# Performance work log

Measured on AMD Instinct MI355X. Metric: run time of the kernel, lower is better.

Reference implementation:

```python
import jax, jax.numpy as jnp
import numpy as np

D_MODEL = 128
D_INNER = 256   # expand=2
D_STATE = 16
DT_RANK = 8     # ceil(128/16)
D_CONV = 2
GROUPS = 4
EPS = 1e-5


def _mamba_dir(x, W_in, conv_w, conv_b, W_x, W_dt, b_dt, A_log, D, W_out):
    # x: [B, L, d_model]
    B, L, _ = x.shape
    xz = x @ W_in                               # [B, L, 2*d_inner]
    xp, z = xz[..., :D_INNER], xz[..., D_INNER:]
    # depthwise causal conv, kernel size 2 (pad-left 1)
    xprev = jnp.pad(xp, ((0, 0), (1, 0), (0, 0)))[:, :L]
    xc = jax.nn.silu(xprev * conv_w[:, 0] + xp * conv_w[:, 1] + conv_b)
    xdb = xc @ W_x                              # [B, L, dt_rank + 2*d_state]
    dt_r = xdb[..., :DT_RANK]
    Bc = xdb[..., DT_RANK:DT_RANK + D_STATE]    # [B, L, d_state]
    Cc = xdb[..., DT_RANK + D_STATE:]           # [B, L, d_state]
    dt = jax.nn.softplus(dt_r @ W_dt + b_dt)    # [B, L, d_inner]
    A = -jnp.exp(A_log)                         # [d_inner, d_state]

    def step(h, inp):
        dt_t, B_t, C_t, x_t = inp               # [B,di], [B,ds], [B,ds], [B,di]
        dA = jnp.exp(dt_t[:, :, None] * A)      # [B, di, ds]
        h = dA * h + (dt_t * x_t)[:, :, None] * B_t[:, None, :]
        y = jnp.einsum('bds,bs->bd', h, C_t)
        return h, y

    h0 = jnp.zeros((B, D_INNER, D_STATE), x.dtype)
    xs = (jnp.moveaxis(dt, 1, 0), jnp.moveaxis(Bc, 1, 0),
          jnp.moveaxis(Cc, 1, 0), jnp.moveaxis(xc, 1, 0))
    _, ys = jax.lax.scan(step, h0, xs)          # ys: [L, B, d_inner]
    y = jnp.moveaxis(ys, 0, 1) + D * xc
    y = y * jax.nn.silu(z)
    return y @ W_out                            # [B, L, d_model]


def _groupnorm_silu(x, gamma, beta):
    B, C, H, W = x.shape
    xg = x.reshape(B, GROUPS, C // GROUPS, H, W)
    mu = xg.mean(axis=(2, 3, 4), keepdims=True)
    var = xg.var(axis=(2, 3, 4), keepdims=True)
    xn = ((xg - mu) * jax.lax.rsqrt(var + EPS)).reshape(B, C, H, W)
    return jax.nn.silu(xn * gamma[None, :, None, None] + beta[None, :, None, None])


def setup_inputs() -> dict:
    key = jax.random.key(0)
    ks = jax.random.split(key, 24)
    s = 0.02
    A_log = jnp.log(jnp.tile(jnp.arange(1, D_STATE + 1, dtype=jnp.float32)[None, :], (D_INNER, 1)))
    inp = {"x": jax.random.normal(ks[0], (4, D_MODEL, 64, 64), jnp.float32)}
    for i, sfx in enumerate(("f", "b")):
        o = 1 + 9 * i
        inp[f"W_in_{sfx}"] = jax.random.normal(ks[o], (D_MODEL, 2 * D_INNER)) * s
        inp[f"conv_w_{sfx}"] = jax.random.normal(ks[o + 1], (D_INNER, D_CONV)) * 0.5
        inp[f"conv_b_{sfx}"] = jnp.zeros((D_INNER,))
        inp[f"W_x_{sfx}"] = jax.random.normal(ks[o + 2], (D_INNER, DT_RANK + 2 * D_STATE)) * s
        inp[f"W_dt_{sfx}"] = jax.random.normal(ks[o + 3], (DT_RANK, D_INNER)) * s
        inp[f"b_dt_{sfx}"] = jnp.full((D_INNER,), -3.0)
        inp[f"A_log_{sfx}"] = A_log
        inp[f"D_{sfx}"] = jnp.ones((D_INNER,))
        inp[f"W_out_{sfx}"] = jax.random.normal(ks[o + 4], (D_INNER, D_MODEL)) * s
    inp["gn_gamma"] = jnp.ones((D_MODEL,))
    inp["gn_beta"] = jnp.zeros((D_MODEL,))
    return inp


def reference(x, W_in_f, conv_w_f, conv_b_f, W_x_f, W_dt_f, b_dt_f, A_log_f, D_f, W_out_f,
              W_in_b, conv_w_b, conv_b_b, W_x_b, W_dt_b, b_dt_b, A_log_b, D_b, W_out_b,
              gn_gamma, gn_beta):
    B, C, H, W = x.shape
    xs = x.transpose(0, 2, 3, 1).reshape(B, H * W, C)
    y_f = _mamba_dir(xs, W_in_f, conv_w_f, conv_b_f, W_x_f, W_dt_f, b_dt_f, A_log_f, D_f, W_out_f)
    xr = xs[:, ::-1]
    y_b = _mamba_dir(xr, W_in_b, conv_w_b, conv_b_b, W_x_b, W_dt_b, b_dt_b, A_log_b, D_b, W_out_b)[:, ::-1]
    y = y_f + y_b                               # bidirectional combine
    y = y.reshape(B, H, W, C).transpose(0, 3, 1, 2)
    y = _groupnorm_silu(y, gn_gamma, gn_beta)
    return y + x
```

## Files before the change

kernel.cpp:

```cpp
#include <hip/hip_runtime.h>

#define Bn 4
#define Ln 4096
#define Cn 128
#define DIn 256
#define NCn 128
#define LCn 32
#define ROWS (Bn*Ln)

typedef short s8v __attribute__((ext_vector_type(8)));
typedef short s4v __attribute__((ext_vector_type(4)));
typedef unsigned short u8v __attribute__((ext_vector_type(8)));
typedef unsigned short u4v __attribute__((ext_vector_type(4)));
typedef float f4v __attribute__((ext_vector_type(4)));
typedef float f2v __attribute__((ext_vector_type(2)));

__device__ __forceinline__ float siluf(float x){ return x / (1.f + __expf(-x)); }
__device__ __forceinline__ unsigned short bfr(float f){
  uint u = __float_as_uint(f);
  return (unsigned short)((u + 0x7fffu + ((u>>16)&1u)) >> 16);
}
__device__ __forceinline__ float bf2f(unsigned short u){ return __uint_as_float(((uint)u)<<16); }

__device__ __forceinline__ void sp_w(float r, float& dtv, float& w){
  float e = __expf(-fabsf(r));
  float rc = 1.f / (1.f + e);
  dtv = fmaxf(r, 0.f) + __logf(1.f + e);
  w = (r > 0.f) ? e * rc : rc;
}

__device__ __forceinline__ int tile_off(int r, int gran, int ghalf){
  return ((r>>4)<<9) + ((r&15)<<5) + (((gran ^ ((r>>1)&3)))<<3) + ghalf;
}

#define SMEMB 18432

__global__ __launch_bounds__(256) void k_g1(const float* __restrict__ x,
    const float* __restrict__ Wf, const float* __restrict__ Wb,
    unsigned short* __restrict__ xpf, unsigned short* __restrict__ xpb,
    unsigned short* __restrict__ zbf, unsigned short* __restrict__ zbb)
{
  const int dir = blockIdx.z;
  const float* __restrict__ W = dir ? Wb : Wf;
  unsigned short* __restrict__ xp = dir ? xpb : xpf;
  unsigned short* __restrict__ zb = dir ? zbb : zbf;
  const int row0 = blockIdx.x * 128;
  const int n0 = blockIdx.y;
  const int b = row0 >> 12;
  const int t0 = row0 & (Ln-1);
  const float* __restrict__ xb = x + (size_t)b * Cn * Ln;

  __shared__ __align__(16) char smem[SMEMB];
  short* Ast = (short*)smem;
  short* Bst = (short*)smem + 8*512;
  float* Te  = (float*)smem;

  const int tid = threadIdx.x;
  const int lane = tid & 63;
  const int wid = tid >> 6;
  const int wr = wid >> 1, wc = wid & 1;
  const int r16 = lane & 15, kg = lane >> 4;

  const int q = tid & 31, kq = tid >> 5;
  const int kbase = 4*kq;
  const int g_true = kq >> 1;
  const int ghalf = (kq & 1) * 4;

  f4v acc[4][4];
  #pragma unroll
  for (int i=0;i<4;++i)
    #pragma unroll
    for (int j=0;j<4;++j) acc[i][j] = (f4v){0.f,0.f,0.f,0.f};

  float4 va[4], vb[4];
  {
    #pragma unroll
    for (int kk=0;kk<4;++kk) {
      va[kk] = (dir==0)
        ? *(const float4*)(xb + (size_t)(kbase+kk)*Ln + t0 + 4*q)
        : *(const float4*)(xb + (size_t)(kbase+kk)*Ln + (Ln-4 - t0 - 4*q));
      vb[kk] = *(const float4*)(W + (size_t)(kbase+kk)*512 + n0*128 + 4*q);
    }
  }
  for (int ks=0; ks<4; ++ks) {
    if (ks) __syncthreads();
    #pragma unroll
    for (int e=0;e<4;++e) {
      int r = 4*q + e;
      int off = tile_off(r, g_true, ghalf);
      int c = dir ? (3-e) : e;
      s4v hv;
      #pragma unroll
      for (int kk=0;kk<4;++kk) hv[kk] = (short)bfr(((const float*)&va[kk])[c]);
      *(s4v*)&Ast[off] = hv;
    }
    #pragma unroll
    for (int e=0;e<4;++e) {
      int r = 4*q + e;
      int off = tile_off(r, g_true, ghalf);
      s4v hv;
      #pragma unroll
      for (int kk=0;kk<4;++kk) hv[kk] = (short)bfr(((const float*)&vb[kk])[e]);
      *(s4v*)&Bst[off] = hv;
    }
    __syncthreads();
    if (ks < 3) {
      const int k0n = (ks+1)*32;
      #pragma unroll
      for (int kk=0;kk<4;++kk) {
        va[kk] = (dir==0)
          ? *(const float4*)(xb + (size_t)(k0n+kbase+kk)*Ln + t0 + 4*q)
          : *(const float4*)(xb + (size_t)(k0n+kbase+kk)*Ln + (Ln-4 - t0 - 4*q));
        vb[kk] = *(const float4*)(W + (size_t)(k0n+kbase+kk)*512 + n0*128 + 4*q);
      }
    }
    const int gsh = ((kg ^ ((r16>>1)&3)) << 3);
    s8v fa[4], fb[4];
    #pragma unroll
    for (int m=0;m<4;++m) fa[m] = *(const s8v*)&Ast[(wr*4+m)*512 + r16*32 + gsh];
    #pragma unroll
    for (int n=0;n<4;++n) fb[n] = *(const s8v*)&Bst[(wc*4+n)*512 + r16*32 + gsh];
    #pragma unroll
    for (int m=0;m<4;++m)
      #pragma unroll
      for (int n=0;n<4;++n)
        acc[m][n] = __builtin_amdgcn_mfma_f32_16x16x32_bf16(fa[m], fb[n], acc[m][n], 0,0,0);
  }
  __syncthreads();
  float* Tw = Te + wid*1088;
  #pragma unroll
  for (int m=0;m<4;++m) {
    #pragma unroll
    for (int n=0;n<4;++n)
      #pragma unroll
      for (int v=0;v<4;++v)
        Tw[(kg*4+v)*68 + n*16 + r16] = acc[m][n][v];
    #pragma unroll
    for (int rr=0;rr<4;++rr) {
      int r = rr*4 + (lane>>4);
      int c4 = lane & 15;
      float4 v4 = *(const float4*)&Tw[r*68 + c4*4];
      int row = row0 + wr*64 + m*16 + r;
      int colL = wc*64 + c4*4;
      u4v u; u[0]=bfr(v4.x); u[1]=bfr(v4.y); u[2]=bfr(v4.z); u[3]=bfr(v4.w);
      if (n0 < 2) {
        *(u4v*)(xp + (size_t)row*256 + n0*128 + colL) = u;
      } else {
        *(u4v*)(zb + (size_t)row*256 + (n0-2)*128 + colL) = u;
      }
    }
  }
}

__global__ __launch_bounds__(256) void k_conv(
    const unsigned short* __restrict__ xpf, const unsigned short* __restrict__ xpb,
    const float* __restrict__ cwf, const float* __restrict__ cwb,
    const float* __restrict__ cbf, const float* __restrict__ cbb,
    unsigned short* __restrict__ xcf, unsigned short* __restrict__ xcb)
{
  const int dir = blockIdx.y;
  const unsigned short* __restrict__ xpd = dir ? xpb : xpf;
  const float* __restrict__ cw = dir ? cwb : cwf;
  const float* __restrict__ cb = dir ? cbb : cbf;
  unsigned short* __restrict__ xc = dir ? xcb : xcf;
  const int n4 = ROWS * 64;
  for (int idx4 = blockIdx.x*256 + threadIdx.x; idx4 < n4; idx4 += gridDim.x*256) {
    int row = idx4 >> 6;
    int d0 = (idx4 & 63) * 4;
    u4v curu = *(const u4v*)(xpd + (size_t)row*256 + d0);
    u4v prevu = (u4v){0,0,0,0};
    if (row & (Ln-1)) prevu = *(const u4v*)(xpd + (size_t)(row-1)*256 + d0);
    float4 cwA = *(const float4*)(cw + d0*2);
    float4 cwB = *(const float4*)(cw + d0*2 + 4);
    float4 cb4 = *(const float4*)(cb + d0);
    u4v r;
    r[0] = bfr(siluf(fmaf(bf2f(prevu[0]),cwA.x, fmaf(bf2f(curu[0]),cwA.y, cb4.x))));
    r[1] = bfr(siluf(fmaf(bf2f(prevu[1]),cwA.z, fmaf(bf2f(curu[1]),cwA.w, cb4.y))));
    r[2] = bfr(siluf(fmaf(bf2f(prevu[2]),cwB.x, fmaf(bf2f(curu[2]),cwB.y, cb4.z))));
    r[3] = bfr(siluf(fmaf(bf2f(prevu[3]),cwB.z, fmaf(bf2f(curu[3]),cwB.w, cb4.w))));
    *(u4v*)(xc + (size_t)row*256 + d0) = r;
  }
}

__global__ __launch_bounds__(256) void k_g2(
    const unsigned short* __restrict__ xcf, const unsigned short* __restrict__ xcb,
    const float* __restrict__ Wxf, const float* __restrict__ Wxb,
    float* __restrict__ xdbf, float* __restrict__ xdbb)
{
  const int dir = blockIdx.z;
  const unsigned short* __restrict__ xc = dir ? xcb : xcf;
  const float* __restrict__ Wx = dir ? Wxb : Wxf;
  float* __restrict__ xdb = dir ? xdbb : xdbf;
  const int row0 = blockIdx.x * 64;

  __shared__ __align__(16) short Ast[4*512];
  __shared__ __align__(16) short Bst[4*512];

  const int tid = threadIdx.x;
  const int lane = tid & 63;
  const int wid = tid >> 6;
  const int wr = wid >> 1, wc = wid & 1;
  const int r16 = lane & 15, kg = lane >> 4;
  const int ar = tid >> 2, ag = tid & 3;
  const int bn = tid & 63, bg = tid >> 6;

  f4v acc[2][2];
  #pragma unroll
  for (int i=0;i<2;++i)
    #pragma unroll
    for (int j=0;j<2;++j) acc[i][j] = (f4v){0.f,0.f,0.f,0.f};

  for (int ks=0; ks<8; ++ks) {
    const int k0 = ks*32;
    if (ks) __syncthreads();
    {
      u8v u = *(const u8v*)(xc + (size_t)(row0+ar)*256 + k0 + ag*8);
      *(u8v*)&Ast[tile_off(ar, ag, 0)] = u;
    }
    {
      s8v hv;
      #pragma unroll
      for (int i=0;i<8;++i) {
        int k = k0 + bg*8 + i;
        float f = (bn < 40) ? Wx[(size_t)k*40 + bn] : 0.f;
        hv[i] = (short)bfr(f);
      }
      *(s8v*)&Bst[tile_off(bn, bg, 0)] = hv;
    }
    __syncthreads();
    const int gsh = ((kg ^ ((r16>>1)&3)) << 3);
    s8v fa[2], fb[2];
    #pragma unroll
    for (int m=0;m<2;++m) fa[m] = *(const s8v*)&Ast[(wr*2+m)*512 + r16*32 + gsh];
    #pragma unroll
    for (int n=0;n<2;++n) fb[n] = *(const s8v*)&Bst[(wc*2+n)*512 + r16*32 + gsh];
    #pragma unroll
    for (int m=0;m<2;++m)
      #pragma unroll
      for (int n=0;n<2;++n)
        acc[m][n] = __builtin_amdgcn_mfma_f32_16x16x32_bf16(fa[m], fb[n], acc[m][n], 0,0,0);
  }
  #pragma unroll
  for (int m=0;m<2;++m)
    #pragma unroll
    for (int n=0;n<2;++n) {
      int col = wc*32 + n*16 + r16;
      if (col < 40) {
        #pragma unroll
        for (int v=0;v<4;++v) {
          int row = row0 + wr*32 + m*16 + kg*4 + v;
          xdb[(size_t)row*40 + col] = acc[m][n][v];
        }
      }
    }
}

__global__ __launch_bounds__(128,4) void k_pass1(
    const float* __restrict__ xdbf, const float* __restrict__ xdbb,
    const unsigned short* __restrict__ xcf, const unsigned short* __restrict__ xcb,
    const float* __restrict__ Wdtf, const float* __restrict__ Wdtb,
    const float* __restrict__ bdtf, const float* __restrict__ bdtb,
    const float* __restrict__ Alf, const float* __restrict__ Alb,
    float* __restrict__ sdtf, float* __restrict__ sdtb,
    float* __restrict__ hkf, float* __restrict__ hkb)
{
  const int dir = blockIdx.y;
  const float* __restrict__ xdb = dir ? xdbb : xdbf;
  const unsigned short* __restrict__ xc = dir ? xcb : xcf;
  const float* __restrict__ Wdt = dir ? Wdtb : Wdtf;
  const float* __restrict__ bdt = dir ? bdtb : bdtf;
  const float* __restrict__ Al  = dir ? Alb  : Alf;
  float* __restrict__ sdt = dir ? sdtb : sdtf;
  float* __restrict__ hk  = dir ? hkb  : hkf;
  const int dh = blockIdx.x & 1;
  const int cc = blockIdx.x >> 1;
  const int b = cc >> 7, c = cc & 127;
  const int t0 = c * LCn;
  __shared__ float S[LCn*32];
  const int tid = threadIdx.x;
  #pragma unroll
  for (int j=0;j<6;++j) {
    int idx = tid + j*128;
    int t = idx/24, jj = idx - t*24;
    S[t*32 + jj] = xdb[(size_t)(b*Ln + t0 + t)*40 + jj];
  }
  const int d = dh*128 + tid;
  float Areg[16];
  bool st = true;
  #pragma unroll
  for (int s=0;s<16;++s) {
    Areg[s] = -__expf(Al[d*16+s]);
    st = st && (fabsf(Areg[s] + (float)(s+1)) <= 3e-5f*(float)(s+1));
  }
  f2v wdt2[4];
  #pragma unroll
  for (int j=0;j<4;++j) wdt2[j] = (f2v){Wdt[(2*j)*256+d], Wdt[(2*j+1)*256+d]};
  const float bd = bdt[d];
  f2v h2[8];
  #pragma unroll
  for (int i=0;i<8;++i) h2[i] = (f2v){0.f,0.f};
  float sacc = 0.f;
  const unsigned short* xcp = xc + (size_t)(b*Ln + t0)*256 + d;
  __syncthreads();
  if (st) {
    for (int t=0;t<LCn;++t) {
      float4 sA = *(const float4*)&S[t*32];
      float4 sB = *(const float4*)&S[t*32+4];
      f2v r2 = (f2v){sA.x,sA.y}*wdt2[0] + (f2v){sA.z,sA.w}*wdt2[1];
      r2 = (f2v){sB.x,sB.y}*wdt2[2] + r2;
      r2 = (f2v){sB.z,sB.w}*wdt2[3] + r2;
      float rr = bd + r2.x + r2.y;
      float dtv, wv;
      sp_w(rr, dtv, wv);
      float4 b0 = *(const float4*)&S[t*32+8];
      float4 b1 = *(const float4*)&S[t*32+12];
      float4 b2 = *(const float4*)&S[t*32+16];
      float4 b3 = *(const float4*)&S[t*32+20];
      float xv = bf2f(xcp[(size_t)t*256]);
      float u = dtv * xv;
      sacc += dtv;
      float w2s = wv*wv;
      float w4 = w2s*w2s, w8 = w4*w4;
      f2v wstep = (f2v){w2s, w2s};
      f2v wpa = (f2v){wv, w2s};
      f2v wpb = wpa * (f2v){w8, w8};
      f2v u2 = (f2v){u, u};
      h2[0] = h2[0]*wpa + u2*(f2v){b0.x,b0.y}; wpa *= wstep;
      h2[4] = h2[4]*wpb + u2*(f2v){b2.x,b2.y}; wpb *= wstep;
      h2[1] = h2[1]*wpa + u2*(f2v){b0.z,b0.w}; wpa *= wstep;
      h2[5] = h2[5]*wpb + u2*(f2v){b2.z,b2.w}; wpb *= wstep;
      h2[2] = h2[2]*wpa + u2*(f2v){b1.x,b1.y}; wpa *= wstep;
      h2[6] = h2[6]*wpb + u2*(f2v){b3.x,b3.y}; wpb *= wstep;
      h2[3] = h2[3]*wpa + u2*(f2v){b1.z,b1.w};
      h2[7] = h2[7]*wpb + u2*(f2v){b3.z,b3.w};
    }
  } else {
    for (int t=0;t<LCn;++t) {
      float4 sA = *(const float4*)&S[t*32];
      float4 sB = *(const float4*)&S[t*32+4];
      float rr = bd;
      rr = fmaf(sA.x,wdt2[0].x, fmaf(sA.y,wdt2[0].y, fmaf(sA.z,wdt2[1].x, fmaf(sA.w,wdt2[1].y, rr))));
      rr = fmaf(sB.x,wdt2[2].x, fmaf(sB.y,wdt2[2].y, fmaf(sB.z,wdt2[3].x, fmaf(sB.w,wdt2[3].y, rr))));
      float dtv, wv;
      sp_w(rr, dtv, wv);
      float bq[16];
      #pragma unroll
      for (int i=0;i<4;++i) *(float4*)&bq[4*i] = *(const float4*)&S[t*32 + 8 + 4*i];
      float xv = bf2f(xcp[(size_t)t*256]);
      float u = dtv * xv;
      sacc += dtv;
      #pragma unroll
      for (int s=0;s<16;++s) {
        float hv = (s&1) ? h2[s>>1].y : h2[s>>1].x;
        hv = fmaf(hv, __expf(dtv*Areg[s]), u*bq[s]);
        if (s&1) h2[s>>1].y = hv; else h2[s>>1].x = hv;
      }
    }
  }
  sdt[(size_t)(b*NCn + c)*256 + d] = sacc;
  #pragma unroll
  for (int i=0;i<8;++i) {
    hk[(size_t)((b*NCn + c)*16 + 2*i)*256 + d]   = h2[i].x;
    hk[(size_t)((b*NCn + c)*16 + 2*i+1)*256 + d] = h2[i].y;
  }
}

__global__ __launch_bounds__(256) void k_pass2(
    const float* __restrict__ Alf, const float* __restrict__ Alb,
    const float* __restrict__ sdtf, const float* __restrict__ sdtb,
    float* __restrict__ hkf, float* __restrict__ hkb)
{
  const int dir = blockIdx.y;
  const float* __restrict__ Al  = dir ? Alb : Alf;
  const float* __restrict__ sdt = dir ? sdtb : sdtf;
  float* __restrict__ hk = dir ? hkb : hkf;
  int g = blockIdx.x*256 + threadIdx.x;
  int d = g & 255, s = (g >> 8) & 15, b = g >> 12;
  float Ad = -__expf(Al[d*16+s]);
  float h = 0.f;
  float sd_n = sdt[(size_t)(b*NCn)*256 + d];
  size_t hi_n = (size_t)((b*NCn)*16 + s)*256 + d;
  float he_n = hk[hi_n];
  for (int c=0;c<NCn;++c) {
    float sd = sd_n, he = he_n;
    size_t hi = hi_n;
    if (c+1 < NCn) {
      int bc = b*NCn + c + 1;
      sd_n = sdt[(size_t)bc*256 + d];
      hi_n = (size_t)(bc*16 + s)*256 + d;
      he_n = hk[hi_n];
    }
    hk[hi] = h;
    h = fmaf(__expf(Ad*sd), h, he);
  }
}

__global__ __launch_bounds__(128,4) void k_pass3(
    const float* __restrict__ xdbf, const float* __restrict__ xdbb,
    const unsigned short* __restrict__ xcf, const unsigned short* __restrict__ xcb,
    const float* __restrict__ Wdtf, const float* __restrict__ Wdtb,
    const float* __restrict__ bdtf, const float* __restrict__ bdtb,
    const float* __restrict__ Alf, const float* __restrict__ Alb,
    const float* __restrict__ Dvf, const float* __restrict__ Dvb,
    const float* __restrict__ hkf, const float* __restrict__ hkb,
    const unsigned short* __restrict__ zbf, const unsigned short* __restrict__ zbb,
    unsigned short* __restrict__ ygf, unsigned short* __restrict__ ygb)
{
  const int dir = blockIdx.y;
  const float* __restrict__ xdb = dir ? xdbb : xdbf;
  const unsigned short* __restrict__ xc = dir ? xcb : xcf;
  const float* __restrict__ Wdt = dir ? Wdtb : Wdtf;
  const float* __restrict__ bdt = dir ? bdtb : bdtf;
  const float* __restrict__ Al  = dir ? Alb  : Alf;
  const float* __restrict__ Dv  = dir ? Dvb  : Dvf;
  const float* __restrict__ hk  = dir ? hkb  : hkf;
  const unsigned short* __restrict__ zbd = dir ? zbb : zbf;
  unsigned short* __restrict__ yg = dir ? ygb : ygf;
  const int dh = blockIdx.x & 1;
  const int cc = blockIdx.x >> 1;
  const int b = cc >> 7, c = cc & 127;
  const int t0 = c * LCn;
  __shared__ float S[LCn*48];
  const int tid = threadIdx.x;
  #pragma unroll
  for (int j=0;j<10;++j) {
    int idx = tid + j*128;
    int t = idx/40, jj = idx - t*40;
    S[t*48 + jj] = xdb[(size_t)(b*Ln + t0 + t)*40 + jj];
  }
  const int d = dh*128 + tid;
  float Areg[16];
  bool st = true;
  #pragma unroll
  for (int s=0;s<16;++s) {
    Areg[s] = -__expf(Al[d*16+s]);
    st = st && (fabsf(Areg[s] + (float)(s+1)) <= 3e-5f*(float)(s+1));
  }
  f2v wdt2[4];
  #pragma unroll
  for (int j=0;j<4;++j) wdt2[j] = (f2v){Wdt[(2*j)*256+d], Wdt[(2*j+1)*256+d]};
  const float bd = bdt[d];
  const float Dd = Dv[d];
  f2v h2[8];
  #pragma unroll
  for (int i=0;i<8;++i)
    h2[i] = (f2v){hk[(size_t)((b*NCn + c)*16 + 2*i)*256 + d],
                  hk[(size_t)((b*NCn + c)*16 + 2*i+1)*256 + d]};
  const unsigned short* xcp = xc + (size_t)(b*Ln + t0)*256 + d;
  const unsigned short* zbp = zbd + (size_t)(b*Ln + t0)*256 + d;
  unsigned short* ygp = yg + (size_t)(b*Ln + t0)*256 + d;
  __syncthreads();
  if (st) {
    for (int t=0;t<LCn;++t) {
      float4 sA = *(const float4*)&S[t*48];
      float4 sB = *(const float4*)&S[t*48+4];
      f2v r2 = (f2v){sA.x,sA.y}*wdt2[0] + (f2v){sA.z,sA.w}*wdt2[1];
      r2 = (f2v){sB.x,sB.y}*wdt2[2] + r2;
      r2 = (f2v){sB.z,sB.w}*wdt2[3] + r2;
      float rr = bd + r2.x + r2.y;
      float dtv, wv;
      sp_w(rr, dtv, wv);
      float4 b0 = *(const float4*)&S[t*48+8];
      float4 b1 = *(const float4*)&S[t*48+12];
      float4 b2 = *(const float4*)&S[t*48+16];
      float4 b3 = *(const float4*)&S[t*48+20];
      float4 c0 = *(const float4*)&S[t*48+24];
      float4 c1 = *(const float4*)&S[t*48+28];
      float4 c2 = *(const float4*)&S[t*48+32];
      float4 c3 = *(const float4*)&S[t*48+36];
      float xv = bf2f(xcp[(size_t)t*256]);
      float u = dtv * xv;
      float w2s = wv*wv;
      float w4 = w2s*w2s, w8 = w4*w4;
      f2v wstep = (f2v){w2s, w2s};
      f2v wpa = (f2v){wv, w2s};
      f2v wpb = wpa * (f2v){w8, w8};
      f2v u2 = (f2v){u, u};
      f2v yA = (f2v){0.f,0.f}, yB = (f2v){0.f,0.f};
      h2[0] = h2[0]*wpa + u2*(f2v){b0.x,b0.y}; yA = h2[0]*(f2v){c0.x,c0.y} + yA; wpa *= wstep;
      h2[4] = h2[4]*wpb + u2*(f2v){b2.x,b2.y}; yB = h2[4]*(f2v){c2.x,c2.y} + yB; wpb *= wstep;
      h2[1] = h2[1]*wpa + u2*(f2v){b0.z,b0.w}; yA = h2[1]*(f2v){c0.z,c0.w} + yA; wpa *= wstep;
      h2[5] = h2[5]*wpb + u2*(f2v){b2.z,b2.w}; yB = h2[5]*(f2v){c2.z,c2.w} + yB; wpb *= wstep;
      h2[2] = h2[2]*wpa + u2*(f2v){b1.x,b1.y}; yA = h2[2]*(f2v){c1.x,c1.y} + yA; wpa *= wstep;
      h2[6] = h2[6]*wpb + u2*(f2v){b3.x,b3.y}; yB = h2[6]*(f2v){c3.x,c3.y} + yB; wpb *= wstep;
      h2[3] = h2[3]*wpa + u2*(f2v){b1.z,b1.w}; yA = h2[3]*(f2v){c1.z,c1.w} + yA;
      h2[7] = h2[7]*wpb + u2*(f2v){b3.z,b3.w}; yB = h2[7]*(f2v){c3.z,c3.w} + yB;
      float y = yA.x + yA.y + yB.x + yB.y;
      y = fmaf(Dd, xv, y);
      float zv = bf2f(zbp[(size_t)t*256]);
      ygp[(size_t)t*256] = bfr(y * siluf(zv));
    }
  } else {
    for (int t=0;t<LCn;++t) {
      float4 sA = *(const float4*)&S[t*48];
      float4 sB = *(const float4*)&S[t*48+4];
      float rr = bd;
      rr = fmaf(sA.x,wdt2[0].x, fmaf(sA.y,wdt2[0].y, fmaf(sA.z,wdt2[1].x, fmaf(sA.w,wdt2[1].y, rr))));
      rr = fmaf(sB.x,wdt2[2].x, fmaf(sB.y,wdt2[2].y, fmaf(sB.z,wdt2[3].x, fmaf(sB.w,wdt2[3].y, rr))));
      float dtv, wv;
      sp_w(rr, dtv, wv);
      float bq[16], cq[16];
      #pragma unroll
      for (int i=0;i<4;++i) {
        *(float4*)&bq[4*i] = *(const float4*)&S[t*48 + 8 + 4*i];
        *(float4*)&cq[4*i] = *(const float4*)&S[t*48 + 24 + 4*i];
      }
      float xv = bf2f(xcp[(size_t)t*256]);
      float u = dtv * xv;
      float y = 0.f;
      #pragma unroll
      for (int s=0;s<16;++s) {
        float hv = (s&1) ? h2[s>>1].y : h2[s>>1].x;
        hv = fmaf(hv, __expf(dtv*Areg[s]), u*bq[s]);
        if (s&1) h2[s>>1].y = hv; else h2[s>>1].x = hv;
        y = fmaf(hv, cq[s], y);
      }
      y = fmaf(Dd, xv, y);
      float zv = bf2f(zbp[(size_t)t*256]);
      ygp[(size_t)t*256] = bfr(y * siluf(zv));
    }
  }
}

__global__ __launch_bounds__(256) void k_gout(
    const unsigned short* __restrict__ ygf, const unsigned short* __restrict__ ygb,
    const float* __restrict__ Wof, const float* __restrict__ Wob,
    float* __restrict__ yp)
{
  const int row0 = blockIdx.x * 64;
  const int khalf = blockIdx.y;
  float* __restrict__ ypart = yp + (size_t)khalf * ROWS * 128;
  const int b = row0 >> 12;
  const int l0 = row0 & (Ln-1);

  __shared__ __align__(16) char smem[SMEMB];
  short* Ast = (short*)smem;
  short* Bst = (short*)smem + 4*512;
  float* Te  = (float*)smem;

  const int tid = threadIdx.x;
  const int lane = tid & 63;
  const int wid = tid >> 6;
  const int wr = wid >> 1, wc = wid & 1;
  const int r16 = lane & 15, kg = lane >> 4;

  const int ar = tid >> 2, ag = tid & 3;
  const int q = tid & 31, kq = tid >> 5;
  const int kbase = 4*kq;
  const int g_true = kq >> 1;
  const int ghalf = (kq & 1) * 4;

  f4v acc[2][4];
  #pragma unroll
  for (int i=0;i<2;++i)
    #pragma unroll
    for (int j=0;j<4;++j) acc[i][j] = (f4v){0.f,0.f,0.f,0.f};

  for (int ks=0; ks<8; ++ks) {
    const int dir = ks >> 2;
    const int kk0 = khalf*128 + (ks & 3)*32;
    const unsigned short* __restrict__ ygd = dir ? ygb : ygf;
    const float* __restrict__ Wod = dir ? Wob : Wof;
    if (ks) __syncthreads();
    {
      int rl = l0 + ar;
      size_t srow = (size_t)b*Ln + (dir ? (Ln-1-rl) : rl);
      u8v u = *(const u8v*)(ygd + srow*256 + kk0 + ag*8);
      *(u8v*)&Ast[tile_off(ar, ag, 0)] = u;
    }
    {
      float4 vb[4];
      #pragma unroll
      for (int kk=0;kk<4;++kk)
        vb[kk] = *(const float4*)(Wod + (size_t)(kk0+kbase+kk)*128 + 4*q);
      #pragma unroll
      for (int e=0;e<4;++e) {
        int r = 4*q + e;
        int off = tile_off(r, g_true, ghalf);
        s4v hv;
        #pragma unroll
        for (int kk=0;kk<4;++kk) hv[kk] = (short)bfr(((const float*)&vb[kk])[e]);
        *(s4v*)&Bst[off] = hv;
      }
    }
    __syncthreads();
    const int gsh = ((kg ^ ((r16>>1)&3)) << 3);
    s8v fa[2], fb[4];
    #pragma unroll
    for (int m=0;m<2;++m) fa[m] = *(const s8v*)&Ast[(wr*2+m)*512 + r16*32 + gsh];
    #pragma unroll
    for (int n=0;n<4;++n) fb[n] = *(const s8v*)&Bst[(wc*4+n)*512 + r16*32 + gsh];
    #pragma unroll
    for (int m=0;m<2;++m)
      #pragma unroll
      for (int n=0;n<4;++n)
        acc[m][n] = __builtin_amdgcn_mfma_f32_16x16x32_bf16(fa[m], fb[n], acc[m][n], 0,0,0);
  }
  __syncthreads();
  float* Tw = Te + wid*1088;
  #pragma unroll
  for (int m=0;m<2;++m) {
    #pragma unroll
    for (int n=0;n<4;++n)
      #pragma unroll
      for (int v=0;v<4;++v)
        Tw[(kg*4+v)*68 + n*16 + r16] = acc[m][n][v];
    #pragma unroll
    for (int rr=0;rr<4;++rr) {
      int r = rr*4 + (lane>>4);
      int c4 = lane & 15;
      float4 v4 = *(const float4*)&Tw[r*68 + c4*4];
      int row = row0 + wr*32 + m*16 + r;
      *(float4*)(ypart + (size_t)row*128 + wc*64 + c4*4) = v4;
    }
    __syncthreads();
  }
}

__global__ __launch_bounds__(256) void k_gnstat(const float* __restrict__ yp,
    float* __restrict__ ysum, float* __restrict__ part)
{
  const int bg = blockIdx.x >> 4;
  const int blk = blockIdx.x & 15;
  const int b = bg >> 2, g = bg & 3;
  const size_t P = (size_t)ROWS*128;
  float s=0.f, q=0.f;
  #pragma unroll
  for (int i=0;i<8;++i) {
    int e4 = blk*2048 + threadIdx.x + i*256;
    int l = e4 >> 3, c4 = e4 & 7;
    size_t base = (size_t)(b*Ln + l)*128 + g*32 + c4*4;
    float4 v0 = *(const float4*)(yp + base);
    float4 v1 = *(const float4*)(yp + P + base);
    float4 v;
    v.x = v0.x+v1.x;
    v.y = v0.y+v1.y;
    v.z = v0.z+v1.z;
    v.w = v0.w+v1.w;
    *(float4*)(ysum + base) = v;
    s += v.x+v.y+v.z+v.w;
    q = fmaf(v.x,v.x, fmaf(v.y,v.y, fmaf(v.z,v.z, fmaf(v.w,v.w, q))));
  }
  __shared__ float rs[256], rq[256];
  rs[threadIdx.x]=s; rq[threadIdx.x]=q;
  __syncthreads();
  for (int off=128; off>0; off>>=1) {
    if (threadIdx.x < off) { rs[threadIdx.x]+=rs[threadIdx.x+off]; rq[threadIdx.x]+=rq[threadIdx.x+off]; }
    __syncthreads();
  }
  if (threadIdx.x==0) { part[blockIdx.x*2]=rs[0]; part[blockIdx.x*2+1]=rq[0]; }
}

__global__ void k_gnred(const float* __restrict__ part, float* __restrict__ mr)
{
  int t = threadIdx.x;
  if (t < 16) {
    float s=0.f,q=0.f;
    for (int k=0;k<16;++k){ s+=part[(t*16+k)*2]; q+=part[(t*16+k)*2+1]; }
    const float inv = 1.f/131072.f;
    float mean = s*inv;
    float var = fmaf(-mean, mean, q*inv);
    mr[t*2] = mean;
    mr[t*2+1] = rsqrtf(var + 1e-5f);
  }
}

__global__ __launch_bounds__(256) void k_gnapply(const float* __restrict__ ysum,
    const float* __restrict__ mr, const float* __restrict__ gamma, const float* __restrict__ beta,
    const float* __restrict__ x, float* __restrict__ out)
{
  const int b = blockIdx.x >> 6;
  const int l0 = (blockIdx.x & 63) * 64;
  __shared__ float T[64][132];
  const int tid = threadIdx.x;
  #pragma unroll
  for (int j=0;j<8;++j) {
    int f = tid + j*256;
    int l = f >> 5, c4 = f & 31;
    *(float4*)&T[l][c4*4] = *(const float4*)(ysum + (size_t)(b*Ln + l0 + l)*128 + c4*4);
  }
  __syncthreads();
  #pragma unroll
  for (int j=0;j<8;++j) {
    int f = tid + j*256;
    int c = f >> 4, lv = f & 15;
    int bg = b*4 + (c>>5);
    float mean = mr[bg*2];
    float rstd = mr[bg*2+1];
    float gam = gamma[c], bet = beta[c];
    size_t base = (size_t)(b*Cn + c)*Ln + l0 + lv*4;
    float4 xv = *(const float4*)(x + base);
    float4 r;
    r.x = siluf(fmaf((T[lv*4+0][c]-mean)*rstd, gam, bet)) + xv.x;
    r.y = siluf(fmaf((T[lv*4+1][c]-mean)*rstd, gam, bet)) + xv.y;
    r.z = siluf(fmaf((T[lv*4+2][c]-mean)*rstd, gam, bet)) + xv.z;
    r.w = siluf(fmaf((T[lv*4+3][c]-mean)*rstd, gam, bet)) + xv.w;
    *(float4*)(out + base) = r;
  }
}

extern "C" void kernel_launch(void* const* d_in, const int* in_sizes, int n_in,
                              void* d_out, int out_size, void* d_ws, size_t ws_size,
                              hipStream_t stream) {
  const float* x      = (const float*)d_in[0];
  const float* W_in_f = (const float*)d_in[1];
  const float* cw_f   = (const float*)d_in[2];
  const float* cb_f   = (const float*)d_in[3];
  const float* Wx_f   = (const float*)d_in[4];
  const float* Wdt_f  = (const float*)d_in[5];
  const float* bdt_f  = (const float*)d_in[6];
  const float* Al_f   = (const float*)d_in[7];
  const float* D_f    = (const float*)d_in[8];
  const float* Wo_f   = (const float*)d_in[9];
  const float* W_in_b = (const float*)d_in[10];
  const float* cw_b   = (const float*)d_in[11];
  const float* cb_b   = (const float*)d_in[12];
  const float* Wx_b   = (const float*)d_in[13];
  const float* Wdt_b  = (const float*)d_in[14];
  const float* bdt_b  = (const float*)d_in[15];
  const float* Al_b   = (const float*)d_in[16];
  const float* D_b    = (const float*)d_in[17];
  const float* Wo_b   = (const float*)d_in[18];
  const float* gamma  = (const float*)d_in[19];
  const float* beta   = (const float*)d_in[20];
  float* out = (float*)d_out;

  float* w = (float*)d_ws;
  size_t o = 0;
  float* xpr0 = w + o; o += (size_t)ROWS*256;
  float* xpr1 = w + o; o += (size_t)ROWS*256;
  unsigned short* xc0 = (unsigned short*)(w + o); o += (size_t)ROWS*128;
  unsigned short* xc1 = (unsigned short*)(w + o); o += (size_t)ROWS*128;
  unsigned short* zb0 = (unsigned short*)(w + o); o += (size_t)ROWS*128;
  unsigned short* zb1 = (unsigned short*)(w + o); o += (size_t)ROWS*128;
  unsigned short* yg0 = (unsigned short*)(w + o); o += (size_t)ROWS*128;
  unsigned short* yg1 = (unsigned short*)(w + o); o += (size_t)ROWS*128;
  float* xdb0 = w + o; o += (size_t)ROWS*40;
  float* xdb1 = w + o; o += (size_t)ROWS*40;
  float* sdt0 = w + o; o += (size_t)Bn*NCn*256;
  float* sdt1 = w + o; o += (size_t)Bn*NCn*256;
  float* hk0  = w + o; o += (size_t)Bn*NCn*16*256;
  float* hk1  = w + o; o += (size_t)Bn*NCn*16*256;
  float* part = w + o; o += 512;
  float* mr   = w + o; o += 32;
  unsigned short* xp0 = (unsigned short*)xpr0;
  unsigned short* xp1 = (unsigned short*)xpr1;
  float* yp   = xpr0;
  float* ysum = xdb0;
  if (ws_size < o*sizeof(float)) return;

  k_g1<<<dim3(ROWS/128, 4, 2), 256, 0, stream>>>(x, W_in_f, W_in_b, xp0, xp1, zb0, zb1);
  k_conv<<<dim3(1024, 2), 256, 0, stream>>>(xp0, xp1, cw_f, cw_b, cb_f, cb_b, xc0, xc1);
  k_g2<<<dim3(ROWS/64, 1, 2), 256, 0, stream>>>(xc0, xc1, Wx_f, Wx_b, xdb0, xdb1);
  k_pass1<<<dim3(Bn*NCn*2, 2), 128, 0, stream>>>(xdb0, xdb1, xc0, xc1, Wdt_f, Wdt_b,
                                                 bdt_f, bdt_b, Al_f, Al_b, sdt0, sdt1, hk0, hk1);
  k_pass2<<<dim3(64, 2), 256, 0, stream>>>(Al_f, Al_b, sdt0, sdt1, hk0, hk1);
  k_pass3<<<dim3(Bn*NCn*2, 2), 128, 0, stream>>>(xdb0, xdb1, xc0, xc1, Wdt_f, Wdt_b,
                                                 bdt_f, bdt_b, Al_f, Al_b, D_f, D_b,
                                                 hk0, hk1, zb0, zb1, yg0, yg1);
  k_gout<<<dim3(ROWS/64, 2), 256, 0, stream>>>(yg0, yg1, Wo_f, Wo_b, yp);
  k_gnstat<<<dim3(256), 256, 0, stream>>>(yp, ysum, part);
  k_gnred<<<dim3(1), 64, 0, stream>>>(part, mr);
  k_gnapply<<<dim3(256), 256, 0, stream>>>(ysum, mr, gamma, beta, x, out);
}
```

Before: 144.9 us.

## Fuse GroupNorm statistics into output GEMM and drop split-K partials

The output projection GEMM now covers the full K dimension of both directions in a single block, removing the two-way split-K. Each block writes the summed result straight to ysum and accumulates per-group sum and sum-of-squares through shared-memory atomics. This eliminates the separate k_gnstat kernel, along with writing and re-reading two full fp32 partial buffers. In exchange the GEMM grid is halved (256 blocks), which lowers parallelism, and each block runs twice as many K steps.

```diff
diff --git a/kernel.cpp b/kernel.cpp
--- a/kernel.cpp
+++ b/kernel.cpp
@@ -525,11 +525,9 @@
 __global__ __launch_bounds__(256) void k_gout(
     const unsigned short* __restrict__ ygf, const unsigned short* __restrict__ ygb,
     const float* __restrict__ Wof, const float* __restrict__ Wob,
-    float* __restrict__ yp)
+    float* __restrict__ ysum, float* __restrict__ part)
 {
   const int row0 = blockIdx.x * 64;
-  const int khalf = blockIdx.y;
-  float* __restrict__ ypart = yp + (size_t)khalf * ROWS * 128;
   const int b = row0 >> 12;
   const int l0 = row0 & (Ln-1);
 
@@ -537,6 +535,7 @@
   short* Ast = (short*)smem;
   short* Bst = (short*)smem + 4*512;
   float* Te  = (float*)smem;
+  __shared__ float gsum[4], gsq[4];
 
   const int tid = threadIdx.x;
   const int lane = tid & 63;
@@ -550,15 +549,17 @@
   const int g_true = kq >> 1;
   const int ghalf = (kq & 1) * 4;
 
+  if (tid < 4) { gsum[tid] = 0.f; gsq[tid] = 0.f; }
+
   f4v acc[2][4];
   #pragma unroll
   for (int i=0;i<2;++i)
     #pragma unroll
     for (int j=0;j<4;++j) acc[i][j] = (f4v){0.f,0.f,0.f,0.f};
 
-  for (int ks=0; ks<8; ++ks) {
-    const int dir = ks >> 2;
-    const int kk0 = khalf*128 + (ks & 3)*32;
+  for (int ks=0; ks<16; ++ks) {
+    const int dir = ks >> 3;
+    const int kk0 = (ks & 7)*32;
     const unsigned short* __restrict__ ygd = dir ? ygb : ygf;
     const float* __restrict__ Wod = dir ? Wob : Wof;
     if (ks) __syncthreads();
@@ -598,6 +599,9 @@
   }
   __syncthreads();
   float* Tw = Te + wid*1088;
+  const int c4 = lane & 15;
+  const int gidx = wc*2 + (c4 >> 3);
+  float ps = 0.f, pq = 0.f;
   #pragma unroll
   for (int m=0;m<2;++m) {
     #pragma unroll
@@ -608,55 +612,33 @@
     #pragma unroll
     for (int rr=0;rr<4;++rr) {
       int r = rr*4 + (lane>>4);
-      int c4 = lane & 15;
       float4 v4 = *(const float4*)&Tw[r*68 + c4*4];
       int row = row0 + wr*32 + m*16 + r;
-      *(float4*)(ypart + (size_t)row*128 + wc*64 + c4*4) = v4;
+      *(float4*)(ysum + (size_t)row*128 + wc*64 + c4*4) = v4;
+      ps += v4.x + v4.y + v4.z + v4.w;
+      pq = fmaf(v4.x,v4.x, fmaf(v4.y,v4.y, fmaf(v4.z,v4.z, fmaf(v4.w,v4.w, pq))));
     }
     __syncthreads();
   }
-}
-
-__global__ __launch_bounds__(256) void k_gnstat(const float* __restrict__ yp,
-    float* __restrict__ ysum, float* __restrict__ part)
-{
-  const int bg = blockIdx.x >> 4;
-  const int blk = blockIdx.x & 15;
-  const int b = bg >> 2, g = bg & 3;
-  const size_t P = (size_t)ROWS*128;
-  float s=0.f, q=0.f;
-  #pragma unroll
-  for (int i=0;i<8;++i) {
-    int e4 = blk*2048 + threadIdx.x + i*256;
-    int l = e4 >> 3, c4 = e4 & 7;
-    size_t base = (size_t)(b*Ln + l)*128 + g*32 + c4*4;
-    float4 v0 = *(const float4*)(yp + base);
-    float4 v1 = *(const float4*)(yp + P + base);
-    float4 v;
-    v.x = v0.x+v1.x;
-    v.y = v0.y+v1.y;
-    v.z = v0.z+v1.z;
-    v.w = v0.w+v1.w;
-    *(float4*)(ysum + base) = v;
-    s += v.x+v.y+v.z+v.w;
-    q = fmaf(v.x,v.x, fmaf(v.y,v.y, fmaf(v.z,v.z, fmaf(v.w,v.w, q))));
-  }
-  __shared__ float rs[256], rq[256];
-  rs[threadIdx.x]=s; rq[threadIdx.x]=q;
+  atomicAdd(&gsum[gidx], ps);
+  atomicAdd(&gsq[gidx], pq);
   __syncthreads();
-  for (int off=128; off>0; off>>=1) {
-    if (threadIdx.x < off) { rs[threadIdx.x]+=rs[threadIdx.x+off]; rq[threadIdx.x]+=rq[threadIdx.x+off]; }
-    __syncthreads();
-  }
-  if (threadIdx.x==0) { part[blockIdx.x*2]=rs[0]; part[blockIdx.x*2+1]=rq[0]; }
+  if (tid < 4) {
+    part[blockIdx.x*8 + tid*2]     = gsum[tid];
+    part[blockIdx.x*8 + tid*2 + 1] = gsq[tid];
+  }
 }
 
 __global__ void k_gnred(const float* __restrict__ part, float* __restrict__ mr)
 {
   int t = threadIdx.x;
   if (t < 16) {
+    int b = t >> 2, g = t & 3;
     float s=0.f,q=0.f;
-    for (int k=0;k<16;++k){ s+=part[(t*16+k)*2]; q+=part[(t*16+k)*2+1]; }
+    for (int blk=0; blk<64; ++blk) {
+      s += part[(b*64+blk)*8 + g*2];
+      q += part[(b*64+blk)*8 + g*2 + 1];
+    }
     const float inv = 1.f/131072.f;
     float mean = s*inv;
     float var = fmaf(-mean, mean, q*inv);
@@ -741,11 +723,10 @@
   float* sdt1 = w + o; o += (size_t)Bn*NCn*256;
   float* hk0  = w + o; o += (size_t)Bn*NCn*16*256;
   float* hk1  = w + o; o += (size_t)Bn*NCn*16*256;
-  float* part = w + o; o += 512;
+  float* part = w + o; o += 2048;
   float* mr   = w + o; o += 32;
   unsigned short* xp0 = (unsigned short*)xpr0;
   unsigned short* xp1 = (unsigned short*)xpr1;
-  float* yp   = xpr0;
   float* ysum = xdb0;
   if (ws_size < o*sizeof(float)) return;
 
@@ -758,8 +739,7 @@
   k_pass3<<<dim3(Bn*NCn*2, 2), 128, 0, stream>>>(xdb0, xdb1, xc0, xc1, Wdt_f, Wdt_b,
                                                  bdt_f, bdt_b, Al_f, Al_b, D_f, D_b,
                                                  hk0, hk1, zb0, zb1, yg0, yg1);
-  k_gout<<<dim3(ROWS/64, 2), 256, 0, stream>>>(yg0, yg1, Wo_f, Wo_b, yp);
-  k_gnstat<<<dim3(256), 256, 0, stream>>>(yp, ysum, part);
+  k_gout<<<dim3(ROWS/64), 256, 0, stream>>>(yg0, yg1, Wo_f, Wo_b, ysum, part);
   k_gnred<<<dim3(1), 64, 0, stream>>>(part, mr);
   k_gnapply<<<dim3(256), 256, 0, stream>>>(ysum, mr, gamma, beta, x, out);
 }
```

After: 146.0 us. About the same (+0.8%).
